# Performance work log

Measured on AMD Instinct MI355X. Metric: run time of the kernel, lower is better.

Reference implementation:

```python
import jax, jax.numpy as jnp
import numpy as np

B, NQ, T, M, DIM, KVD, H, DH = 8, 256, 32, 256, 768, 1024, 8, 64
INNER = H * DH
EPS = 1e-5  # torch LayerNorm default


def _layernorm(z, g, b):
    mu = jnp.mean(z, axis=-1, keepdims=True)
    var = jnp.mean(jnp.square(z - mu), axis=-1, keepdims=True)
    return (z - mu) * jax.lax.rsqrt(var + EPS) * g + b


def setup_inputs() -> dict:
    key = jax.random.key(0)
    ks = jax.random.split(key, 6)
    x = jax.random.normal(ks[0], (B, NQ, DIM), dtype=jnp.float32)
    k_v = jax.random.normal(ks[1], (B, T, M, KVD), dtype=jnp.float32)
    # LayerNorm affine params (torch init: weight=1, bias=0)
    g_q = jnp.ones((DIM,), jnp.float32)
    b_q = jnp.zeros((DIM,), jnp.float32)
    g_kv = jnp.ones((KVD,), jnp.float32)
    b_kv = jnp.zeros((KVD,), jnp.float32)
    # Linear weights (no bias); stored as [in, out] for x @ W
    Wq = jax.random.normal(ks[2], (DIM, INNER), dtype=jnp.float32) * 0.02
    Wkv = jax.random.normal(ks[3], (KVD, 2 * INNER), dtype=jnp.float32) * 0.02
    Wo = jax.random.normal(ks[4], (INNER, DIM), dtype=jnp.float32) * 0.02
    return {"x": x, "k_v": k_v, "g_q": g_q, "b_q": b_q, "g_kv": g_kv,
            "b_kv": b_kv, "Wq": Wq, "Wkv": Wkv, "Wo": Wo}


def reference(x, k_v, g_q, b_q, g_kv, b_kv, Wq, Wkv, Wo):
    scale = DH ** -0.5
    xq = _layernorm(x, g_q, b_q)                       # [b, nq, dim]
    kv = _layernorm(k_v, g_kv, b_kv)                   # [b, t, m, kvd]
    kv = kv.reshape(kv.shape[0], -1, kv.shape[-1])     # [b, tm, kvd]
    q = xq @ Wq                                        # [b, nq, inner]
    kvp = kv @ Wkv                                     # [b, tm, 2*inner]
    k, v = jnp.split(kvp, 2, axis=-1)
    # b n (h d) -> b h n d
    def heads(z):
        return z.reshape(z.shape[0], z.shape[1], H, DH).transpose(0, 2, 1, 3)
    q, k, v = heads(q) * scale, heads(k), heads(v)
    sim = jnp.einsum('bhid,bhjd->bhij', q, k)          # [b, h, nq, tm]
    sim = sim - jax.lax.stop_gradient(jnp.max(sim, axis=-1, keepdims=True))
    attn = jax.nn.softmax(sim, axis=-1)
    out = jnp.einsum('bhij,bhjd->bhid', attn, v)       # [b, h, nq, dh]
    out = out.transpose(0, 2, 1, 3).reshape(out.shape[0], NQ, INNER)
    return out @ Wo                                    # [b, nq, dim]
```

## Files before the change

kernel.cpp:

```cpp
#include <hip/hip_runtime.h>
#include <math.h>

#define NB     8
#define NQX    256
#define TMX    8192
#define DIMX   768
#define KVDX   1024
#define NHX    8
#define DHX    64
#define INNERX 512
#define NSPLIT 8

typedef __bf16 bf16x8 __attribute__((ext_vector_type(8)));
typedef float  f32x4  __attribute__((ext_vector_type(4)));

__device__ inline ushort f2bf(float f) {
    uint u = __float_as_uint(f);
    return (ushort)((u + 0x7FFFu + ((u >> 16) & 1u)) >> 16);
}

template<int COLS>
__global__ __launch_bounds__(256)
void ln_apply_bf16_kernel(const float* __restrict__ in, const float* __restrict__ g,
                          const float* __restrict__ bet, ushort* __restrict__ out)
{
    const int wid  = threadIdx.x >> 6;
    const int lane = threadIdx.x & 63;
    const long row = (long)blockIdx.x * 4 + wid;
    const float4* p4 = (const float4*)(in + row * COLS);
    float4 v[COLS / 256];
    float s = 0.f, ss = 0.f;
#pragma unroll
    for (int c = 0; c < COLS / 256; ++c) {
        v[c] = p4[c * 64 + lane];
        s  += v[c].x + v[c].y + v[c].z + v[c].w;
        ss += v[c].x * v[c].x + v[c].y * v[c].y + v[c].z * v[c].z + v[c].w * v[c].w;
    }
#pragma unroll
    for (int off = 1; off < 64; off <<= 1) {
        s  += __shfl_xor(s,  off, 64);
        ss += __shfl_xor(ss, off, 64);
    }
    const float m  = s * (1.f / COLS);
    const float rs = rsqrtf(ss * (1.f / COLS) - m * m + 1e-5f);
    ushort* orow = out + row * COLS;
#pragma unroll
    for (int c = 0; c < COLS / 256; ++c) {
        float4 gg = ((const float4*)g)[c * 64 + lane];
        float4 bb = ((const float4*)bet)[c * 64 + lane];
        uint2 pk;
        pk.x = f2bf((v[c].x - m) * rs * gg.x + bb.x)
             | ((uint)f2bf((v[c].y - m) * rs * gg.y + bb.y) << 16);
        pk.y = f2bf((v[c].z - m) * rs * gg.z + bb.z)
             | ((uint)f2bf((v[c].w - m) * rs * gg.w + bb.w) << 16);
        *(uint2*)(orow + (c * 64 + lane) * 4) = pk;
    }
}

__global__ __launch_bounds__(256)
void transpose_bf16_kernel(const float* __restrict__ in, ushort* __restrict__ out,
                           int K, int N)
{
    __shared__ float tile[64][65];
    const int t  = threadIdx.x;
    const int n0 = blockIdx.x * 64, k0 = blockIdx.y * 64;
#pragma unroll
    for (int i = 0; i < 16; ++i) {
        int f = i * 256 + t, r = f >> 6, c = f & 63;
        tile[r][c] = in[(size_t)(k0 + r) * N + n0 + c];
    }
    __syncthreads();
#pragma unroll
    for (int i = 0; i < 16; ++i) {
        int f = i * 256 + t, r = f >> 6, c = f & 63;
        out[(size_t)(n0 + r) * K + k0 + c] = f2bf(tile[c][r]);
    }
}

__global__ __launch_bounds__(256)
void gemm_f32_kernel(const float* __restrict__ A, const float* __restrict__ W,
                     float* __restrict__ C, int M, int N, int K)
{
    __shared__ float As[16][132];
    __shared__ float Bs[16][132];
    const int t  = threadIdx.x;
    const int bm = blockIdx.y * 128;
    const int bn = blockIdx.x * 128;
    const int ty = t >> 4, tx = t & 15;
    const int ar = t >> 1, ak0 = (t & 1) * 8;
    const int bk = t >> 4, bn0 = (t & 15) * 8;

    float acc[8][8];
#pragma unroll
    for (int i = 0; i < 8; ++i)
#pragma unroll
        for (int j = 0; j < 8; ++j) acc[i][j] = 0.f;

    const float* Arow = A + (size_t)(bm + ar) * K;

    for (int k0 = 0; k0 < K; k0 += 16) {
        float4 a0 = *(const float4*)(Arow + k0 + ak0);
        float4 a1 = *(const float4*)(Arow + k0 + ak0 + 4);
        const float* Wrow = W + (size_t)(k0 + bk) * N + bn + bn0;
        float4 w0 = *(const float4*)(Wrow);
        float4 w1 = *(const float4*)(Wrow + 4);

        __syncthreads();
        As[ak0 + 0][ar] = a0.x;
        As[ak0 + 1][ar] = a0.y;
        As[ak0 + 2][ar] = a0.z;
        As[ak0 + 3][ar] = a0.w;
        As[ak0 + 4][ar] = a1.x;
        As[ak0 + 5][ar] = a1.y;
        As[ak0 + 6][ar] = a1.z;
        As[ak0 + 7][ar] = a1.w;
        *(float4*)&Bs[bk][bn0]     = w0;
        *(float4*)&Bs[bk][bn0 + 4] = w1;
        __syncthreads();

#pragma unroll
        for (int kk = 0; kk < 16; ++kk) {
            float a[8], b[8];
            *(float4*)&a[0] = *(const float4*)&As[kk][ty * 8];
            *(float4*)&a[4] = *(const float4*)&As[kk][ty * 8 + 4];
            *(float4*)&b[0] = *(const float4*)&Bs[kk][tx * 8];
            *(float4*)&b[4] = *(const float4*)&Bs[kk][tx * 8 + 4];
#pragma unroll
            for (int i = 0; i < 8; ++i)
#pragma unroll
                for (int j = 0; j < 8; ++j)
                    acc[i][j] = fmaf(a[i], b[j], acc[i][j]);
        }
    }

#pragma unroll
    for (int i = 0; i < 8; ++i) {
        float* Crow = C + (size_t)(bm + ty * 8 + i) * N + bn + tx * 8;
        *(float4*)Crow       = make_float4(acc[i][0], acc[i][1], acc[i][2], acc[i][3]);
        *(float4*)(Crow + 4) = make_float4(acc[i][4], acc[i][5], acc[i][6], acc[i][7]);
    }
}

template<bool SWZ>
__global__ __launch_bounds__(256)
void mfma_gemm_bt(const ushort* __restrict__ A, const ushort* __restrict__ Bt,
                  ushort* __restrict__ C, int M, int N, int K, float escale)
{
    __shared__ ushort As[128 * 32];
    __shared__ ushort Bs[128 * 32];
    const int t    = threadIdx.x;
    const int wid  = t >> 6, lane = t & 63;
    const int lr   = lane & 15, quad = lane >> 4;
    const int wq   = wid >> 1, wn = wid & 1;

    int mt_i, nt_i;
    if (SWZ) {
        int flat = blockIdx.x + (int)(gridDim.x * blockIdx.y);
        mt_i = ((flat >> 6) << 3) | (flat & 7);
        nt_i = (flat >> 3) & 7;
    } else {
        mt_i = blockIdx.y; nt_i = blockIdx.x;
    }
    const int bm = mt_i * 128, bn = nt_i * 128;

    f32x4 acc[4][4];
#pragma unroll
    for (int i = 0; i < 4; ++i)
#pragma unroll
        for (int j = 0; j < 4; ++j) acc[i][j] = (f32x4)(0.f);

    for (int k0 = 0; k0 < K; k0 += 32) {
        __syncthreads();
#pragma unroll
        for (int o = 0; o < 2; ++o) {
            int s  = o * 256 + t;
            int n  = s >> 2;
            int kc = (s & 3) ^ ((n >> 2) & 3);
            const ushort* ga = A  + (size_t)(bm + n) * K + k0 + kc * 8;
            const ushort* gb = Bt + (size_t)(bn + n) * K + k0 + kc * 8;
            __builtin_amdgcn_global_load_lds(
                (const __attribute__((address_space(1))) void*)ga,
                (__attribute__((address_space(3))) void*)(&As[0] + o * 2048 + wid * 512),
                16, 0, 0);
            __builtin_amdgcn_global_load_lds(
                (const __attribute__((address_space(1))) void*)gb,
                (__attribute__((address_space(3))) void*)(&Bs[0] + o * 2048 + wid * 512),
                16, 0, 0);
        }
        __syncthreads();

        bf16x8 af[4], bfr[4];
#pragma unroll
        for (int mt = 0; mt < 4; ++mt) {
            int rn = wq * 64 + mt * 16 + lr;
            af[mt] = *(const bf16x8*)&As[rn * 32 + (quad ^ ((rn >> 2) & 3)) * 8];
        }
#pragma unroll
        for (int nt = 0; nt < 4; ++nt) {
            int rn = wn * 64 + nt * 16 + lr;
            bfr[nt] = *(const bf16x8*)&Bs[rn * 32 + (quad ^ ((rn >> 2) & 3)) * 8];
        }
#pragma unroll
        for (int mt = 0; mt < 4; ++mt)
#pragma unroll
            for (int nt = 0; nt < 4; ++nt)
                acc[mt][nt] = __builtin_amdgcn_mfma_f32_16x16x32_bf16(
                    af[mt], bfr[nt], acc[mt][nt], 0, 0, 0);
    }

#pragma unroll
    for (int mt = 0; mt < 4; ++mt)
#pragma unroll
        for (int nt = 0; nt < 4; ++nt) {
            int row = bm + wq * 64 + mt * 16 + quad * 4;
            int col = bn + wn * 64 + nt * 16 + lr;
#pragma unroll
            for (int r = 0; r < 4; ++r)
                C[(size_t)(row + r) * N + col] = f2bf(acc[mt][nt][r] * escale);
        }
}

__global__ __launch_bounds__(256)
void attn_mfma_kernel(const ushort* __restrict__ qbuf, const ushort* __restrict__ kvp,
                      float* __restrict__ po, float* __restrict__ pl)
{
    __shared__ ushort Ks[64][72];
    __shared__ ushort Vt[64][72];
    __shared__ ushort Ps[128][72];
    const int t    = threadIdx.x;
    const int w    = t >> 6, lane = t & 63;
    const int lr   = lane & 15, quad = lane >> 4;
    const int qt   = blockIdx.x;
    const int h    = blockIdx.y;
    const int z    = blockIdx.z;
    const int b    = z >> 3, sp = z & 7;

#pragma unroll
    for (int i = 0; i < 4; ++i) {
        int idx = i * 256 + t;
        int row = idx >> 3, c8 = (idx & 7) * 8;
        const ushort* src = qbuf + (size_t)(b * NQX + qt * 128 + row) * INNERX + h * DHX + c8;
        *(uint4*)&Ps[row][c8] = *(const uint4*)src;
    }
    __syncthreads();
    bf16x8 qf[2][2];
#pragma unroll
    for (int mt = 0; mt < 2; ++mt)
#pragma unroll
        for (int ks = 0; ks < 2; ++ks)
            qf[mt][ks] = *(const bf16x8*)&Ps[w * 32 + mt * 16 + lr][ks * 32 + quad * 8];
    __syncthreads();

    f32x4 O[2][4];
    float l_[2][4];
#pragma unroll
    for (int mt = 0; mt < 2; ++mt) {
#pragma unroll
        for (int nt = 0; nt < 4; ++nt) O[mt][nt] = (f32x4)(0.f);
#pragma unroll
        for (int r = 0; r < 4; ++r) l_[mt][r] = 0.f;
    }

    const size_t kvrow0 = (size_t)b * TMX * KVDX + (size_t)(sp * (TMX / NSPLIT)) * KVDX + h * DHX;
    const int vp = t & 31, vdg = t >> 5;

    for (int jt = 0; jt < (TMX / NSPLIT) / 64; ++jt) {
        const ushort* kb = kvp + kvrow0 + (size_t)jt * 64 * KVDX;
        const ushort* kp = kb + (size_t)(t >> 3) * KVDX + (t & 7) * 8;
        uint4 kd0 = *(const uint4*)(kp);
        uint4 kd1 = *(const uint4*)(kp + 32 * KVDX);
        const ushort* vbp = kb + 512 + (size_t)(2 * vp) * KVDX + vdg * 8;
        uint4 vd0 = *(const uint4*)(vbp);
        uint4 vd1 = *(const uint4*)(vbp + KVDX);

        __syncthreads();
        *(uint4*)&Ks[t >> 3][(t & 7) * 8]        = kd0;
        *(uint4*)&Ks[32 + (t >> 3)][(t & 7) * 8] = kd1;
        const uint* v0w = (const uint*)&vd0;
        const uint* v1w = (const uint*)&vd1;
#pragma unroll
        for (int e = 0; e < 8; ++e) {
            uint u0 = (e & 1) ? (v0w[e >> 1] >> 16) : (v0w[e >> 1] & 0xFFFFu);
            uint u1 = (e & 1) ? (v1w[e >> 1] >> 16) : (v1w[e >> 1] & 0xFFFFu);
            *(uint*)&Vt[vdg * 8 + e][2 * vp] = u0 | (u1 << 16);
        }
        __syncthreads();

#pragma unroll
        for (int mt = 0; mt < 2; ++mt) {
            f32x4 s[4];
#pragma unroll
            for (int nt = 0; nt < 4; ++nt) s[nt] = (f32x4)(0.f);
#pragma unroll
            for (int ks = 0; ks < 2; ++ks) {
                bf16x8 kf[4];
#pragma unroll
                for (int nt = 0; nt < 4; ++nt)
                    kf[nt] = *(const bf16x8*)&Ks[nt * 16 + lr][ks * 32 + quad * 8];
#pragma unroll
                for (int nt = 0; nt < 4; ++nt)
                    s[nt] = __builtin_amdgcn_mfma_f32_16x16x32_bf16(
                        qf[mt][ks], kf[nt], s[nt], 0, 0, 0);
            }
#pragma unroll
            for (int r = 0; r < 4; ++r) {
                float p0 = __expf(s[0][r]);
                float p1 = __expf(s[1][r]);
                float p2 = __expf(s[2][r]);
                float p3 = __expf(s[3][r]);
                l_[mt][r] += p0 + p1 + p2 + p3;
                int prow = w * 32 + mt * 16 + quad * 4 + r;
                Ps[prow][lr]      = f2bf(p0);
                Ps[prow][16 + lr] = f2bf(p1);
                Ps[prow][32 + lr] = f2bf(p2);
                Ps[prow][48 + lr] = f2bf(p3);
            }
        }

#pragma unroll
        for (int ks = 0; ks < 2; ++ks) {
            bf16x8 vf[4];
#pragma unroll
            for (int nt = 0; nt < 4; ++nt)
                vf[nt] = *(const bf16x8*)&Vt[nt * 16 + lr][ks * 32 + quad * 8];
#pragma unroll
            for (int mt = 0; mt < 2; ++mt) {
                bf16x8 pf = *(const bf16x8*)&Ps[w * 32 + mt * 16 + lr][ks * 32 + quad * 8];
#pragma unroll
                for (int nt = 0; nt < 4; ++nt)
                    O[mt][nt] = __builtin_amdgcn_mfma_f32_16x16x32_bf16(
                        pf, vf[nt], O[mt][nt], 0, 0, 0);
            }
        }
    }

#pragma unroll
    for (int mt = 0; mt < 2; ++mt)
#pragma unroll
        for (int r = 0; r < 4; ++r) {
            float lv = l_[mt][r];
            lv += __shfl_xor(lv, 1, 64);
            lv += __shfl_xor(lv, 2, 64);
            lv += __shfl_xor(lv, 4, 64);
            lv += __shfl_xor(lv, 8, 64);
            int grow = b * NQX + qt * 128 + w * 32 + mt * 16 + quad * 4 + r;
            float* dst = po + (size_t)(sp * 2048 + grow) * INNERX + h * DHX;
#pragma unroll
            for (int nt = 0; nt < 4; ++nt)
                dst[nt * 16 + lr] = O[mt][nt][r];
            if (lr == 0)
                pl[(sp * 2048 + grow) * NHX + h] = lv;
        }
}

__global__ __launch_bounds__(256)
void combine_kernel(const float* __restrict__ po, const float* __restrict__ pl,
                    float* __restrict__ ao)
{
    int idx = blockIdx.x * 256 + threadIdx.x;
    int row = idx >> 7;
    int col = (idx & 127) * 4;
    int h   = col >> 6;
    float L = 0.f;
#pragma unroll
    for (int s = 0; s < NSPLIT; ++s)
        L += pl[(s * 2048 + row) * NHX + h];
    float rL = 1.f / L;
    float4 r = make_float4(0.f, 0.f, 0.f, 0.f);
#pragma unroll
    for (int s = 0; s < NSPLIT; ++s) {
        float4 a = *(const float4*)(po + (size_t)(s * 2048 + row) * INNERX + col);
        r.x += a.x; r.y += a.y; r.z += a.z; r.w += a.w;
    }
    r.x *= rL; r.y *= rL; r.z *= rL; r.w *= rL;
    *(float4*)(ao + (size_t)row * INNERX + col) = r;
}

extern "C" void kernel_launch(void* const* d_in, const int* in_sizes, int n_in,
                              void* d_out, int out_size, void* d_ws, size_t ws_size,
                              hipStream_t stream)
{
    (void)in_sizes; (void)n_in; (void)out_size; (void)ws_size;
    const float* x    = (const float*)d_in[0];
    const float* k_v  = (const float*)d_in[1];
    const float* g_q  = (const float*)d_in[2];
    const float* b_q  = (const float*)d_in[3];
    const float* g_kv = (const float*)d_in[4];
    const float* b_kv = (const float*)d_in[5];
    const float* Wq   = (const float*)d_in[6];
    const float* Wkv  = (const float*)d_in[7];
    const float* Wo   = (const float*)d_in[8];
    float* out = (float*)d_out;

    float* ws       = (float*)d_ws;
    float*  pl      = ws;
    ushort* qbuf    = (ushort*)(ws + 131072);
    float*  ao      = ws + 131072;
    ushort* Wkvt    = (ushort*)(ws + 1179648);
    ushort* xln     = (ushort*)(ws + 1703936);
    ushort* Wqt     = (ushort*)(ws + 1703936 + 786432);
    ushort* kvln    = (ushort*)(ws + 1703936);
    float*  po      = ws + 1703936;
    ushort* kvp     = (ushort*)(ws + 35258368);

    ln_apply_bf16_kernel<DIMX><<<(NB * NQX) / 4, 256, 0, stream>>>(x, g_q, b_q, xln);
    transpose_bf16_kernel<<<dim3(INNERX / 64, DIMX / 64), 256, 0, stream>>>(
        Wq, Wqt, DIMX, INNERX);
    mfma_gemm_bt<false><<<dim3(INNERX / 128, (NB * NQX) / 128), 256, 0, stream>>>(
        xln, Wqt, qbuf, NB * NQX, INNERX, DIMX, 0.125f);

    ln_apply_bf16_kernel<KVDX><<<(NB * TMX) / 4, 256, 0, stream>>>(k_v, g_kv, b_kv, kvln);
    transpose_bf16_kernel<<<dim3((2 * INNERX) / 64, KVDX / 64), 256, 0, stream>>>(
        Wkv, Wkvt, KVDX, 2 * INNERX);
    mfma_gemm_bt<true><<<dim3((2 * INNERX) / 128, (NB * TMX) / 128), 256, 0, stream>>>(
        kvln, Wkvt, kvp, NB * TMX, 2 * INNERX, KVDX, 1.f);

    attn_mfma_kernel<<<dim3(NQX / 128, NHX, NB * NSPLIT), 256, 0, stream>>>(
        qbuf, kvp, po, pl);

    combine_kernel<<<1024, 256, 0, stream>>>(po, pl, ao);
    gemm_f32_kernel<<<dim3(DIMX / 128, (NB * NQX) / 128), 256, 0, stream>>>(
        ao, Wo, out, NB * NQX, DIMX, INNERX);
}
```

Before: 754.6 us.

## Use 256x256-tile 512-thread MFMA GEMM with 4-stage LDS pipeline for KV projection

Replaces the 128x128-tile KV projection GEMM with a new kernel that computes a 256x256 output tile per 512-thread block. Operand tiles are loaded straight into a 4-buffer LDS ring with global_load_lds, using swizzled segments and vmcnt-based waits. The grid is remapped across XCDs and MFMA sections run at raised wave priority. The aim is more reuse per loaded byte and better overlap of loads with compute for the largest GEMM. In exchange it uses more LDS and registers per block, which lowers occupancy, and it relies on hand-written waitcnt logic.

```diff
diff --git a/kernel.cpp b/kernel.cpp
--- a/kernel.cpp
+++ b/kernel.cpp
@@ -220,6 +220,117 @@
         }
 }
 
+__global__ __launch_bounds__(512, 2)
+void mfma_gemm_bt256(const ushort* __restrict__ A, const ushort* __restrict__ Bt,
+                     ushort* __restrict__ C, int M, int N, int K, float escale)
+{
+    __shared__ __attribute__((aligned(16))) ushort As[4 * 8192];
+    __shared__ __attribute__((aligned(16))) ushort Bs[4 * 8192];
+    const int t    = threadIdx.x;
+    const int wid  = t >> 6, lane = t & 63;
+    const int lr   = lane & 15, quad = lane >> 4;
+    const int wm   = wid >> 2, wn = wid & 3;
+
+    const int nbn = N >> 8;
+    {
+    }
+    const int nwg = (int)gridDim.x;
+    const int swq = nwg >> 3, swr = nwg & 7;
+    const int xcd = (int)blockIdx.x & 7, lid = (int)blockIdx.x >> 3;
+    const int swzf = (xcd < swr ? xcd * (swq + 1) : swr * (swq + 1) + (xcd - swr) * swq) + lid;
+    const int bm = (swzf / nbn) * 256, bn = (swzf % nbn) * 256;
+
+    const int srow = t >> 2;
+    const int sseg = (t & 3) ^ ((srow >> 1) & 3);
+    const ushort* gA = A  + (size_t)(bm + srow) * K + sseg * 8;
+    const ushort* gB = Bt + (size_t)(bn + srow) * K + sseg * 8;
+    const size_t rstep = (size_t)128 * K;
+    const int ld0 = wid * 512;
+    const int ld1 = 4096 + wid * 512;
+
+#define STG256(arr, gp, tt) do {                                               \
+        const int _b = (tt) & 3;                                               \
+        const ushort* _g = (gp) + (size_t)(tt) * 32;                           \
+        __builtin_amdgcn_global_load_lds(                                      \
+            (const __attribute__((address_space(1))) void*)_g,                 \
+            (__attribute__((address_space(3))) void*)(arr + _b * 8192 + ld0),  \
+            16, 0, 0);                                                         \
+        __builtin_amdgcn_global_load_lds(                                      \
+            (const __attribute__((address_space(1))) void*)(_g + rstep),       \
+            (__attribute__((address_space(3))) void*)(arr + _b * 8192 + ld1),  \
+            16, 0, 0);                                                         \
+    } while (0)
+
+    const int NT = K >> 5;
+    STG256(As, gA, 0); STG256(Bs, gB, 0);
+    STG256(As, gA, 1); STG256(Bs, gB, 1);
+    STG256(As, gA, 2); STG256(Bs, gB, 2);
+
+    f32x4 acc[8][4];
+#pragma unroll
+    for (int i = 0; i < 8; ++i)
+#pragma unroll
+        for (int j = 0; j < 4; ++j) acc[i][j] = (f32x4)(0.f);
+
+    const int rseg8 = (quad ^ ((lr >> 1) & 3)) * 8;
+    const int aoff = (wm * 128 + lr) * 32 + rseg8;
+    const int boff = (wn * 64 + lr) * 32 + rseg8;
+
+    for (int tt = 0; tt < NT; ++tt) {
+        const int b = tt & 3;
+        if (tt + 2 < NT)      asm volatile("s_waitcnt vmcnt(8)" ::: "memory");
+        else if (tt + 1 < NT) asm volatile("s_waitcnt vmcnt(4)" ::: "memory");
+        else                  asm volatile("s_waitcnt vmcnt(0)" ::: "memory");
+        __builtin_amdgcn_s_barrier();
+        asm volatile("" ::: "memory");
+
+        const ushort* Ab = As + b * 8192 + aoff;
+        const ushort* Bb = Bs + b * 8192 + boff;
+
+        if (tt + 3 < NT) STG256(As, gA, tt + 3);
+        bf16x8 bfr[4], af[4];
+#pragma unroll
+        for (int n = 0; n < 4; ++n)
+            bfr[n] = *(const bf16x8*)(Bb + n * 512);
+#pragma unroll
+        for (int m = 0; m < 4; ++m)
+            af[m] = *(const bf16x8*)(Ab + m * 512);
+        __builtin_amdgcn_s_setprio(1);
+#pragma unroll
+        for (int m = 0; m < 4; ++m)
+#pragma unroll
+            for (int n = 0; n < 4; ++n)
+                acc[m][n] = __builtin_amdgcn_mfma_f32_16x16x32_bf16(
+                    af[m], bfr[n], acc[m][n], 0, 0, 0);
+        __builtin_amdgcn_s_setprio(0);
+
+        if (tt + 3 < NT) STG256(Bs, gB, tt + 3);
+#pragma unroll
+        for (int m = 0; m < 4; ++m)
+            af[m] = *(const bf16x8*)(Ab + (m + 4) * 512);
+        __builtin_amdgcn_s_setprio(1);
+#pragma unroll
+        for (int m = 0; m < 4; ++m)
+#pragma unroll
+            for (int n = 0; n < 4; ++n)
+                acc[m + 4][n] = __builtin_amdgcn_mfma_f32_16x16x32_bf16(
+                    af[m], bfr[n], acc[m + 4][n], 0, 0, 0);
+        __builtin_amdgcn_s_setprio(0);
+    }
+#undef STG256
+
+#pragma unroll
+    for (int m = 0; m < 8; ++m)
+#pragma unroll
+        for (int n = 0; n < 4; ++n) {
+            int row = bm + wm * 128 + m * 16 + quad * 4;
+            int col = bn + wn * 64 + n * 16 + lr;
+#pragma unroll
+            for (int r = 0; r < 4; ++r)
+                C[(size_t)(row + r) * N + col] = f2bf(acc[m][n][r] * escale);
+        }
+}
+
 __global__ __launch_bounds__(256)
 void attn_mfma_kernel(const ushort* __restrict__ qbuf, const ushort* __restrict__ kvp,
                       float* __restrict__ po, float* __restrict__ pl)
@@ -412,7 +523,7 @@
     ln_apply_bf16_kernel<KVDX><<<(NB * TMX) / 4, 256, 0, stream>>>(k_v, g_kv, b_kv, kvln);
     transpose_bf16_kernel<<<dim3((2 * INNERX) / 64, KVDX / 64), 256, 0, stream>>>(
         Wkv, Wkvt, KVDX, 2 * INNERX);
-    mfma_gemm_bt<true><<<dim3((2 * INNERX) / 128, (NB * TMX) / 128), 256, 0, stream>>>(
+    mfma_gemm_bt256<<<dim3((NB * TMX / 256) * ((2 * INNERX) / 256)), 512, 0, stream>>>(
         kvln, Wkvt, kvp, NB * TMX, 2 * INNERX, KVDX, 1.f);
 
     attn_mfma_kernel<<<dim3(NQX / 128, NHX, NB * NSPLIT), 256, 0, stream>>>(
```

New measurement: 730.4 us. -3.2%, faster.

## Use 256x256 pipelined MFMA GEMM for KV projection and bf16 MFMA for output projection

Applied to the files above, without the earlier changes.

Replaces the 128x128 KV projection GEMM with a 512-thread 256x256-tile kernel that double-buffers LDS via direct global-to-LDS loads, interleaves MFMA with loads across barriers, and swizzles workgroups across XCDs. The output projection moves from an fp32 FMA GEMM to a bf16 MFMA GEMM: the combine kernel now emits bf16 and Wo is transposed to bf16. The aim is to cut time in the dominant KV GEMM and the scalar fp32 output GEMM. The trade-off is reduced precision in the output projection and higher register and LDS pressure in the big kernel.

```diff
diff --git a/kernel.cpp b/kernel.cpp
--- a/kernel.cpp
+++ b/kernel.cpp
@@ -74,70 +74,6 @@
     for (int i = 0; i < 16; ++i) {
         int f = i * 256 + t, r = f >> 6, c = f & 63;
         out[(size_t)(n0 + r) * K + k0 + c] = f2bf(tile[c][r]);
-    }
-}
-
-__global__ __launch_bounds__(256)
-void gemm_f32_kernel(const float* __restrict__ A, const float* __restrict__ W,
-                     float* __restrict__ C, int M, int N, int K)
-{
-    __shared__ float As[16][132];
-    __shared__ float Bs[16][132];
-    const int t  = threadIdx.x;
-    const int bm = blockIdx.y * 128;
-    const int bn = blockIdx.x * 128;
-    const int ty = t >> 4, tx = t & 15;
-    const int ar = t >> 1, ak0 = (t & 1) * 8;
-    const int bk = t >> 4, bn0 = (t & 15) * 8;
-
-    float acc[8][8];
-#pragma unroll
-    for (int i = 0; i < 8; ++i)
-#pragma unroll
-        for (int j = 0; j < 8; ++j) acc[i][j] = 0.f;
-
-    const float* Arow = A + (size_t)(bm + ar) * K;
-
-    for (int k0 = 0; k0 < K; k0 += 16) {
-        float4 a0 = *(const float4*)(Arow + k0 + ak0);
-        float4 a1 = *(const float4*)(Arow + k0 + ak0 + 4);
-        const float* Wrow = W + (size_t)(k0 + bk) * N + bn + bn0;
-        float4 w0 = *(const float4*)(Wrow);
-        float4 w1 = *(const float4*)(Wrow + 4);
-
-        __syncthreads();
-        As[ak0 + 0][ar] = a0.x;
-        As[ak0 + 1][ar] = a0.y;
-        As[ak0 + 2][ar] = a0.z;
-        As[ak0 + 3][ar] = a0.w;
-        As[ak0 + 4][ar] = a1.x;
-        As[ak0 + 5][ar] = a1.y;
-        As[ak0 + 6][ar] = a1.z;
-        As[ak0 + 7][ar] = a1.w;
-        *(float4*)&Bs[bk][bn0]     = w0;
-        *(float4*)&Bs[bk][bn0 + 4] = w1;
-        __syncthreads();
-
-#pragma unroll
-        for (int kk = 0; kk < 16; ++kk) {
-            float a[8], b[8];
-            *(float4*)&a[0] = *(const float4*)&As[kk][ty * 8];
-            *(float4*)&a[4] = *(const float4*)&As[kk][ty * 8 + 4];
-            *(float4*)&b[0] = *(const float4*)&Bs[kk][tx * 8];
-            *(float4*)&b[4] = *(const float4*)&Bs[kk][tx * 8 + 4];
-#pragma unroll
-            for (int i = 0; i < 8; ++i)
-#pragma unroll
-                for (int j = 0; j < 8; ++j)
-                    acc[i][j] = fmaf(a[i], b[j], acc[i][j]);
-        }
-    }
-
-#pragma unroll
-    for (int i = 0; i < 8; ++i) {
-        float* Crow = C + (size_t)(bm + ty * 8 + i) * N + bn + tx * 8;
-        *(float4*)Crow       = make_float4(acc[i][0], acc[i][1], acc[i][2], acc[i][3]);
-        *(float4*)(Crow + 4) = make_float4(acc[i][4], acc[i][5], acc[i][6], acc[i][7]);
     }
 }
 
@@ -221,6 +157,246 @@
 }
 
 __global__ __launch_bounds__(256)
+void mfma_gemm_bt_f32(const ushort* __restrict__ A, const ushort* __restrict__ Bt,
+                      float* __restrict__ C, int M, int N, int K)
+{
+    __shared__ ushort As[128 * 32];
+    __shared__ ushort Bs[128 * 32];
+    const int t    = threadIdx.x;
+    const int wid  = t >> 6, lane = t & 63;
+    const int lr   = lane & 15, quad = lane >> 4;
+    const int wq   = wid >> 1, wn = wid & 1;
+    const int bm = blockIdx.y * 128, bn = blockIdx.x * 128;
+
+    f32x4 acc[4][4];
+#pragma unroll
+    for (int i = 0; i < 4; ++i)
+#pragma unroll
+        for (int j = 0; j < 4; ++j) acc[i][j] = (f32x4)(0.f);
+
+    for (int k0 = 0; k0 < K; k0 += 32) {
+        __syncthreads();
+#pragma unroll
+        for (int o = 0; o < 2; ++o) {
+            int s  = o * 256 + t;
+            int n  = s >> 2;
+            int kc = (s & 3) ^ ((n >> 2) & 3);
+            const ushort* ga = A  + (size_t)(bm + n) * K + k0 + kc * 8;
+            const ushort* gb = Bt + (size_t)(bn + n) * K + k0 + kc * 8;
+            __builtin_amdgcn_global_load_lds(
+                (const __attribute__((address_space(1))) void*)ga,
+                (__attribute__((address_space(3))) void*)(&As[0] + o * 2048 + wid * 512),
+                16, 0, 0);
+            __builtin_amdgcn_global_load_lds(
+                (const __attribute__((address_space(1))) void*)gb,
+                (__attribute__((address_space(3))) void*)(&Bs[0] + o * 2048 + wid * 512),
+                16, 0, 0);
+        }
+        __syncthreads();
+
+        bf16x8 af[4], bfr[4];
+#pragma unroll
+        for (int mt = 0; mt < 4; ++mt) {
+            int rn = wq * 64 + mt * 16 + lr;
+            af[mt] = *(const bf16x8*)&As[rn * 32 + (quad ^ ((rn >> 2) & 3)) * 8];
+        }
+#pragma unroll
+        for (int nt = 0; nt < 4; ++nt) {
+            int rn = wn * 64 + nt * 16 + lr;
+            bfr[nt] = *(const bf16x8*)&Bs[rn * 32 + (quad ^ ((rn >> 2) & 3)) * 8];
+        }
+#pragma unroll
+        for (int mt = 0; mt < 4; ++mt)
+#pragma unroll
+            for (int nt = 0; nt < 4; ++nt)
+                acc[mt][nt] = __builtin_amdgcn_mfma_f32_16x16x32_bf16(
+                    af[mt], bfr[nt], acc[mt][nt], 0, 0, 0);
+    }
+
+#pragma unroll
+    for (int mt = 0; mt < 4; ++mt)
+#pragma unroll
+        for (int nt = 0; nt < 4; ++nt) {
+            int row = bm + wq * 64 + mt * 16 + quad * 4;
+            int col = bn + wn * 64 + nt * 16 + lr;
+#pragma unroll
+            for (int r = 0; r < 4; ++r)
+                C[(size_t)(row + r) * N + col] = acc[mt][nt][r];
+        }
+}
+
+__global__ __launch_bounds__(512, 2)
+void mfma_gemm_bt256(const ushort* __restrict__ A, const ushort* __restrict__ Bt,
+                     ushort* __restrict__ C, int M, int N, int K, float escale)
+{
+    __shared__ __attribute__((aligned(16))) ushort As[2 * 16384];
+    __shared__ __attribute__((aligned(16))) ushort Bs[2 * 16384];
+    const int t    = threadIdx.x;
+    const int wid  = t >> 6, lane = t & 63;
+    const int lr   = lane & 15, quad = lane >> 4;
+    const int wm   = wid >> 2, wn = wid & 3;
+
+    const int nbn = N >> 8;
+    const int nwg = (int)gridDim.x;
+    const int swq = nwg >> 3, swr = nwg & 7;
+    const int xcd = (int)blockIdx.x & 7, lid = (int)blockIdx.x >> 3;
+    const int swzf = (xcd < swr ? xcd * (swq + 1) : swr * (swq + 1) + (xcd - swr) * swq) + lid;
+    const int bm = (swzf / nbn) * 256, bn = (swzf % nbn) * 256;
+
+    const int slot0 = t, slot1 = 512 + t;
+    const int r0 = slot0 >> 3, p0 = slot0 & 7;
+    const int r1 = slot1 >> 3, p1 = slot1 & 7;
+    const ushort* gA0 = A  + (size_t)(bm + r0) * K + (p0 ^ (r0 & 7)) * 8;
+    const ushort* gA1 = A  + (size_t)(bm + r1) * K + (p1 ^ (r1 & 7)) * 8;
+    const ushort* gB0 = Bt + (size_t)(bn + r0) * K + (p0 ^ (r0 & 7)) * 8;
+    const ushort* gB1 = Bt + (size_t)(bn + r1) * K + (p1 ^ (r1 & 7)) * 8;
+    const size_t hstep = (size_t)128 * K;
+
+#define STGA(tt, h) do {                                                          \
+        const int _l = ((tt) & 1) * 16384 + (h) * 8192;                           \
+        const size_t _g = (size_t)(h) * hstep + (size_t)(tt) * 64;                \
+        __builtin_amdgcn_global_load_lds(                                         \
+            (const __attribute__((address_space(1))) void*)(gA0 + _g),            \
+            (__attribute__((address_space(3))) void*)(As + _l + slot0 * 8),       \
+            16, 0, 0);                                                            \
+        __builtin_amdgcn_global_load_lds(                                         \
+            (const __attribute__((address_space(1))) void*)(gA1 + _g),            \
+            (__attribute__((address_space(3))) void*)(As + _l + slot1 * 8),       \
+            16, 0, 0);                                                            \
+    } while (0)
+#define STGB(tt, h) do {                                                          \
+        const int _l = ((tt) & 1) * 16384 + (h) * 8192;                           \
+        const size_t _g = (size_t)(h) * hstep + (size_t)(tt) * 64;                \
+        __builtin_amdgcn_global_load_lds(                                         \
+            (const __attribute__((address_space(1))) void*)(gB0 + _g),            \
+            (__attribute__((address_space(3))) void*)(Bs + _l + slot0 * 8),       \
+            16, 0, 0);                                                            \
+        __builtin_amdgcn_global_load_lds(                                         \
+            (const __attribute__((address_space(1))) void*)(gB1 + _g),            \
+            (__attribute__((address_space(3))) void*)(Bs + _l + slot1 * 8),       \
+            16, 0, 0);                                                            \
+    } while (0)
+
+    const int aoffr = (wm * 128 + lr) * 64;
+    const int boffr = (wn * 64 + lr) * 64;
+    const int seg0  = (quad ^ (lr & 7)) * 8;
+    const int seg1  = seg0 ^ 32;
+#define LDSA(dd, ah, mi, ks) (*(const bf16x8*)&As[(dd) * 16384 + aoffr + ((ah) * 64 + (mi) * 16) * 64 + ((ks) ? seg1 : seg0)])
+#define LDSB(dd, nf, ks)     (*(const bf16x8*)&Bs[(dd) * 16384 + boffr + (nf) * 1024 + ((ks) ? seg1 : seg0)])
+
+    const int NT = K >> 6;
+
+    STGB(0, 0); STGB(0, 1); STGA(0, 0); STGA(0, 1);
+    STGB(1, 0); STGB(1, 1);
+
+    f32x4 acc[8][4];
+#pragma unroll
+    for (int i = 0; i < 8; ++i)
+#pragma unroll
+        for (int j = 0; j < 4; ++j) acc[i][j] = (f32x4)(0.f);
+
+    bf16x8 Af[8], Bf[8];
+
+    asm volatile("s_waitcnt vmcnt(4)" ::: "memory");
+    __builtin_amdgcn_s_barrier();
+    asm volatile("" ::: "memory");
+#pragma unroll
+    for (int mi = 0; mi < 4; ++mi) {
+        Af[mi * 2 + 0] = LDSA(0, 0, mi, 0);
+        Af[mi * 2 + 1] = LDSA(0, 0, mi, 1);
+    }
+    Bf[0] = LDSB(0, 0, 0); Bf[1] = LDSB(0, 0, 1);
+    Bf[2] = LDSB(0, 1, 0); Bf[3] = LDSB(0, 1, 1);
+
+#define MF4x2(ar, nb) do {                                                        \
+        __builtin_amdgcn_s_setprio(1);                                            \
+        _Pragma("unroll")                                                         \
+        for (int mi = 0; mi < 4; ++mi)                                            \
+            _Pragma("unroll")                                                     \
+            for (int ni = 0; ni < 2; ++ni) {                                      \
+                acc[(ar) + mi][(nb) * 2 + ni] =                                   \
+                    __builtin_amdgcn_mfma_f32_16x16x32_bf16(                      \
+                        Af[mi * 2 + 0], Bf[(nb) * 4 + ni * 2 + 0],                \
+                        acc[(ar) + mi][(nb) * 2 + ni], 0, 0, 0);                  \
+                acc[(ar) + mi][(nb) * 2 + ni] =                                   \
+                    __builtin_amdgcn_mfma_f32_16x16x32_bf16(                      \
+                        Af[mi * 2 + 1], Bf[(nb) * 4 + ni * 2 + 1],                \
+                        acc[(ar) + mi][(nb) * 2 + ni], 0, 0, 0);                  \
+            }                                                                     \
+        __builtin_amdgcn_s_setprio(0);                                            \
+    } while (0)
+
+#define TILE_BODY(tt, dd) do {                                                    \
+                                                \
+        MF4x2(0, 0);                                                              \
+        Bf[4] = LDSB(dd, 2, 0); Bf[5] = LDSB(dd, 2, 1);                           \
+        Bf[6] = LDSB(dd, 3, 0); Bf[7] = LDSB(dd, 3, 1);                           \
+        if ((tt) + 1 < NT) STGA((tt) + 1, 0);                                     \
+        if ((tt) + 2 < NT) asm volatile("s_waitcnt vmcnt(6)" ::: "memory");       \
+        else               asm volatile("s_waitcnt vmcnt(0)" ::: "memory");       \
+        __builtin_amdgcn_s_barrier();                                             \
+        asm volatile("" ::: "memory");                                            \
+                                                \
+        MF4x2(0, 1);                                                              \
+        _Pragma("unroll")                                                         \
+        for (int mi = 0; mi < 4; ++mi) {                                          \
+            Af[mi * 2 + 0] = LDSA(dd, 1, mi, 0);                                  \
+            Af[mi * 2 + 1] = LDSA(dd, 1, mi, 1);                                  \
+        }                                                                         \
+        if ((tt) + 1 < NT) STGA((tt) + 1, 1);                                     \
+        if ((tt) + 2 < NT) asm volatile("s_waitcnt vmcnt(6)" ::: "memory");       \
+        else               asm volatile("s_waitcnt vmcnt(0)" ::: "memory");       \
+        __builtin_amdgcn_s_barrier();                                             \
+        asm volatile("" ::: "memory");                                            \
+                                                \
+        MF4x2(4, 0);                                                              \
+        if ((tt) + 1 < NT) {                                                      \
+            Bf[0] = LDSB((dd) ^ 1, 0, 0); Bf[1] = LDSB((dd) ^ 1, 0, 1);           \
+            Bf[2] = LDSB((dd) ^ 1, 1, 0); Bf[3] = LDSB((dd) ^ 1, 1, 1);           \
+        }                                                                         \
+        if ((tt) + 2 < NT) STGB((tt) + 2, 0);                                     \
+        if ((tt) + 2 < NT) asm volatile("s_waitcnt vmcnt(4)" ::: "memory");       \
+        else               asm volatile("s_waitcnt vmcnt(0)" ::: "memory");       \
+        __builtin_amdgcn_s_barrier();                                             \
+        asm volatile("" ::: "memory");                                            \
+                                                \
+        MF4x2(4, 1);                                                              \
+        if ((tt) + 1 < NT) {                                                      \
+            _Pragma("unroll")                                                     \
+            for (int mi = 0; mi < 4; ++mi) {                                      \
+                Af[mi * 2 + 0] = LDSA((dd) ^ 1, 0, mi, 0);                        \
+                Af[mi * 2 + 1] = LDSA((dd) ^ 1, 0, mi, 1);                        \
+            }                                                                     \
+        }                                                                         \
+        if ((tt) + 2 < NT) STGB((tt) + 2, 1);                                     \
+        __builtin_amdgcn_s_barrier();                                             \
+        asm volatile("" ::: "memory");                                            \
+    } while (0)
+
+    for (int tt = 0; tt < NT; tt += 2) {
+        TILE_BODY(tt, 0);
+        TILE_BODY(tt + 1, 1);
+    }
+#undef TILE_BODY
+#undef MF4x2
+#undef LDSA
+#undef LDSB
+#undef STGA
+#undef STGB
+
+#pragma unroll
+    for (int m = 0; m < 8; ++m)
+#pragma unroll
+        for (int n = 0; n < 4; ++n) {
+            int row = bm + wm * 128 + m * 16 + quad * 4;
+            int col = bn + wn * 64 + n * 16 + lr;
+#pragma unroll
+            for (int r = 0; r < 4; ++r)
+                C[(size_t)(row + r) * N + col] = f2bf(acc[m][n][r] * escale);
+        }
+}
+
+__global__ __launch_bounds__(256)
 void attn_mfma_kernel(const ushort* __restrict__ qbuf, const ushort* __restrict__ kvp,
                       float* __restrict__ po, float* __restrict__ pl)
 {
@@ -355,7 +531,7 @@
 
 __global__ __launch_bounds__(256)
 void combine_kernel(const float* __restrict__ po, const float* __restrict__ pl,
-                    float* __restrict__ ao)
+                    ushort* __restrict__ ao)
 {
     int idx = blockIdx.x * 256 + threadIdx.x;
     int row = idx >> 7;
@@ -372,8 +548,10 @@
         float4 a = *(const float4*)(po + (size_t)(s * 2048 + row) * INNERX + col);
         r.x += a.x; r.y += a.y; r.z += a.z; r.w += a.w;
     }
-    r.x *= rL; r.y *= rL; r.z *= rL; r.w *= rL;
-    *(float4*)(ao + (size_t)row * INNERX + col) = r;
+    uint2 pk;
+    pk.x = f2bf(r.x * rL) | ((uint)f2bf(r.y * rL) << 16);
+    pk.y = f2bf(r.z * rL) | ((uint)f2bf(r.w * rL) << 16);
+    *(uint2*)(ao + (size_t)row * INNERX + col) = pk;
 }
 
 extern "C" void kernel_launch(void* const* d_in, const int* in_sizes, int n_in,
@@ -395,30 +573,33 @@
     float* ws       = (float*)d_ws;
     float*  pl      = ws;
     ushort* qbuf    = (ushort*)(ws + 131072);
-    float*  ao      = ws + 131072;
+    ushort* ao_bf   = (ushort*)(ws + 131072);
     ushort* Wkvt    = (ushort*)(ws + 1179648);
     ushort* xln     = (ushort*)(ws + 1703936);
     ushort* Wqt     = (ushort*)(ws + 1703936 + 786432);
     ushort* kvln    = (ushort*)(ws + 1703936);
     float*  po      = ws + 1703936;
     ushort* kvp     = (ushort*)(ws + 35258368);
+    ushort* Wot     = (ushort*)(ws + 68812800);
 
     ln_apply_bf16_kernel<DIMX><<<(NB * NQX) / 4, 256, 0, stream>>>(x, g_q, b_q, xln);
     transpose_bf16_kernel<<<dim3(INNERX / 64, DIMX / 64), 256, 0, stream>>>(
         Wq, Wqt, DIMX, INNERX);
+    transpose_bf16_kernel<<<dim3(DIMX / 64, INNERX / 64), 256, 0, stream>>>(
+        Wo, Wot, INNERX, DIMX);
     mfma_gemm_bt<false><<<dim3(INNERX / 128, (NB * NQX) / 128), 256, 0, stream>>>(
         xln, Wqt, qbuf, NB * NQX, INNERX, DIMX, 0.125f);
 
     ln_apply_bf16_kernel<KVDX><<<(NB * TMX) / 4, 256, 0, stream>>>(k_v, g_kv, b_kv, kvln);
     transpose_bf16_kernel<<<dim3((2 * INNERX) / 64, KVDX / 64), 256, 0, stream>>>(
         Wkv, Wkvt, KVDX, 2 * INNERX);
-    mfma_gemm_bt<true><<<dim3((2 * INNERX) / 128, (NB * TMX) / 128), 256, 0, stream>>>(
+    mfma_gemm_bt256<<<dim3((NB * TMX / 256) * ((2 * INNERX) / 256)), 512, 0, stream>>>(
         kvln, Wkvt, kvp, NB * TMX, 2 * INNERX, KVDX, 1.f);
 
     attn_mfma_kernel<<<dim3(NQX / 128, NHX, NB * NSPLIT), 256, 0, stream>>>(
         qbuf, kvp, po, pl);
 
-    combine_kernel<<<1024, 256, 0, stream>>>(po, pl, ao);
-    gemm_f32_kernel<<<dim3(DIMX / 128, (NB * NQX) / 128), 256, 0, stream>>>(
-        ao, Wo, out, NB * NQX, DIMX, INNERX);
-}
+    combine_kernel<<<1024, 256, 0, stream>>>(po, pl, ao_bf);
+    mfma_gemm_bt_f32<<<dim3(DIMX / 128, (NB * NQX) / 128), 256, 0, stream>>>(
+        ao_bf, Wot, out, NB * NQX, DIMX, INNERX);
+}
```

Result: faster. 660.6 us (-12.5%).
